# Performance work log

Measured on AMD Instinct MI355X. Metric: run time of the kernel, lower is better.

The kernel has to match this reference:

```python
import jax, jax.numpy as jnp
import numpy as np

B, N, DIM = 4, 4096, 1024
HEADS, DIM_HEAD, M = 16, 64, 128
DIM_INNER = HEADS * DIM_HEAD
SCALE = DIM_HEAD ** -0.5


def setup_inputs() -> dict:
    key = jax.random.key(0)
    ks = jax.random.split(key, 7)
    x = jax.random.normal(ks[0], (B, N, DIM), dtype=jnp.float32)
    mask = jax.random.bernoulli(ks[1], 0.9, (B, N))  # bool [b, n]
    W_qkv = jax.random.normal(ks[2], (DIM, 3 * DIM_INNER), dtype=jnp.float32) * (DIM ** -0.5)
    agent_tokens = jax.random.normal(ks[3], (HEADS, M, DIM_HEAD), dtype=jnp.float32) * 0.02
    W_qa = jax.random.normal(ks[4], (HEADS, HEADS), dtype=jnp.float32) * (HEADS ** -0.5)
    W_ak = jax.random.normal(ks[5], (HEADS, HEADS), dtype=jnp.float32) * (HEADS ** -0.5)
    W_out = jax.random.normal(ks[6], (DIM_INNER, DIM), dtype=jnp.float32) * (DIM_INNER ** -0.5)
    return {"x": x, "mask": mask, "W_qkv": W_qkv, "agent_tokens": agent_tokens,
            "W_qa": W_qa, "W_ak": W_ak, "W_out": W_out}


def reference(x, mask, W_qkv, agent_tokens, W_qa, W_ak, W_out):
    b, n, _ = x.shape
    h, m, d = agent_tokens.shape
    # qkv projection -> [3, b, h, n, d]  (layout matches 'b n (qkv h d)')
    qkv = (x @ W_qkv).reshape(b, n, 3, h, d).transpose(2, 0, 3, 1, 4)
    q, k, v = qkv[0], qkv[1], qkv[2]
    a = agent_tokens * SCALE  # [h, m, d]
    # stage 1: query-agent similarities [b, h, n, m]
    qa_sim = jnp.einsum('bhid,hjd->bhij', q, a)
    # stage 2: agent-key similarities [b, h, m, n]
    ak_sim = jnp.einsum('hid,bhjd->bhij', a, k)
    max_neg = -jnp.finfo(ak_sim.dtype).max
    ak_sim = jnp.where(mask[:, None, None, :], ak_sim, max_neg)
    qa_attn = jax.nn.softmax(qa_sim, axis=-1)
    ak_attn = jax.nn.softmax(ak_sim, axis=-1)
    # talking heads: 1x1 conv over head dim == head-mixing matmul
    qa_attn = jnp.einsum('gh,bhij->bgij', W_qa, qa_attn)
    ak_attn = jnp.einsum('gh,bhij->bgij', W_ak, ak_attn)
    agent_out = jnp.einsum('bhmn,bhnd->bhmd', ak_attn, v)    # [b, h, m, d]
    out = jnp.einsum('bhnm,bhmd->bhnd', qa_attn, agent_out)  # [b, h, n, d]
    out = jnp.where(mask[:, None, :, None], out, 0.0)
    out = out.transpose(0, 2, 1, 3).reshape(b, n, h * d)
    return out @ W_out
```

## Files before the change

kernel.cpp:

```cpp
#include <hip/hip_runtime.h>
#include <stdint.h>

#define DEVI __device__ __forceinline__

typedef __bf16 bf16x8 __attribute__((ext_vector_type(8)));
typedef float  f32x4  __attribute__((ext_vector_type(4)));
typedef unsigned int u32x2 __attribute__((ext_vector_type(2)));
typedef unsigned int u32x4 __attribute__((ext_vector_type(4)));


DEVI unsigned short f2bf(float f) {
  union { float f; unsigned int u; } c; c.f = f;
  return (unsigned short)((c.u + 0x7fffu + ((c.u >> 16) & 1u)) >> 16);
}
DEVI float bf2f(unsigned short s) {
  union { unsigned int u; float f; } c; c.u = ((unsigned int)s) << 16;
  return c.f;
}
DEVI u32x2 pack4(float a, float b, float c, float d) {
  u32x2 r;
  r.x = (unsigned)f2bf(a) | ((unsigned)f2bf(b) << 16);
  r.y = (unsigned)f2bf(c) | ((unsigned)f2bf(d) << 16);
  return r;
}
DEVI bf16x8 ldg8(const unsigned short* p) { return *(const bf16x8*)p; }

DEVI void g2l16(const void* g, void* l) {
  __builtin_amdgcn_global_load_lds(
      (const __attribute__((address_space(1))) unsigned int*)g,
      (__attribute__((address_space(3))) unsigned int*)l, 16, 0, 0);
}

#define MFMA16(acc, a, b) acc = __builtin_amdgcn_mfma_f32_16x16x32_bf16((a), (b), (acc), 0, 0, 0)

__global__ __launch_bounds__(256) void k_prep(
    const float* __restrict__ x, const float* __restrict__ Wqkv,
    const float* __restrict__ ag, const float* __restrict__ Wout,
    unsigned short* __restrict__ Xb, unsigned short* __restrict__ WqkvT,
    unsigned short* __restrict__ Ab, unsigned short* __restrict__ WoT)
{
  __shared__ float ldsT[32][33];
  const int tid = threadIdx.x;
  int bx = blockIdx.x;
  if (bx < 16384) {
    size_t i4 = ((size_t)bx * 256 + tid) * 4;
    f32x4 v = *(const f32x4*)&x[i4];
    *(u32x2*)&Xb[i4] = pack4(v[0], v[1], v[2], v[3]);
    return;
  }
  bx -= 16384;
  if (bx < 3072) {
    int jt = bx % 96, kt = bx / 96;
    int r32 = tid >> 3, c4 = (tid & 7) * 4;
    f32x4 v = *(const f32x4*)&Wqkv[(size_t)(kt * 32 + r32) * 3072 + jt * 32 + c4];
#pragma unroll
    for (int i = 0; i < 4; i++) ldsT[r32][c4 + i] = v[i];
    __syncthreads();
    float o0 = ldsT[c4 + 0][r32], o1 = ldsT[c4 + 1][r32];
    float o2 = ldsT[c4 + 2][r32], o3 = ldsT[c4 + 3][r32];
    *(u32x2*)&WqkvT[(size_t)(jt * 32 + r32) * 1024 + kt * 32 + c4] = pack4(o0, o1, o2, o3);
    return;
  }
  bx -= 3072;
  if (bx < 128) {
    size_t i4 = ((size_t)bx * 256 + tid) * 4;
    f32x4 v = *(const f32x4*)&ag[i4];
    *(u32x2*)&Ab[i4] = pack4(v[0] * 0.125f, v[1] * 0.125f, v[2] * 0.125f, v[3] * 0.125f);
    return;
  }
  bx -= 128;
  {
    int ct = bx % 32, dt = bx / 32;
    int r32 = tid >> 3, c4 = (tid & 7) * 4;
    f32x4 v = *(const f32x4*)&Wout[(size_t)(dt * 32 + r32) * 1024 + ct * 32 + c4];
#pragma unroll
    for (int i = 0; i < 4; i++) ldsT[r32][c4 + i] = v[i];
    __syncthreads();
    float o0 = ldsT[c4 + 0][r32], o1 = ldsT[c4 + 1][r32];
    float o2 = ldsT[c4 + 2][r32], o3 = ldsT[c4 + 3][r32];
    *(u32x2*)&WoT[(size_t)(ct * 32 + r32) * 1024 + dt * 32 + c4] = pack4(o0, o1, o2, o3);
  }
}

__global__ __launch_bounds__(256, 2) void k_gemm_qkv(
    const unsigned short* __restrict__ A, const unsigned short* __restrict__ Bt,
    unsigned short* __restrict__ Q, unsigned short* __restrict__ Kd,
    unsigned short* __restrict__ Vt)
{
  __shared__ __align__(16) unsigned short lA[4096];
  __shared__ __align__(16) unsigned short lB[4096];
  const int tid = threadIdx.x, lane = tid & 63, w = tid >> 6;
  const int q = lane >> 4, r = lane & 15, wr = w >> 1, wc = w & 1;
  const int row0 = blockIdx.y * 128, col0 = blockIdx.x * 128;
  const bool qk = blockIdx.x < 16;
  const int c1 = w, c2 = w + 4;
  const int sr1 = c1 * 16 + (lane >> 2), sr2 = c2 * 16 + (lane >> 2);
  const int sk = 8 * (lane & 3);
  const unsigned short* gA1 = A + (size_t)(row0 + sr1) * 1024 + sk;
  const unsigned short* gA2 = A + (size_t)(row0 + sr2) * 1024 + sk;
  const unsigned short* gB1 = Bt + (size_t)(col0 + sr1) * 1024 + sk;
  const unsigned short* gB2 = Bt + (size_t)(col0 + sr2) * 1024 + sk;
  const unsigned short* sA = qk ? lB : lA;
  const unsigned short* sB = qk ? lA : lB;
  f32x4 acc[4][4];
  const f32x4 z = {0.f, 0.f, 0.f, 0.f};
#pragma unroll
  for (int i = 0; i < 4; i++)
#pragma unroll
    for (int j = 0; j < 4; j++) acc[i][j] = z;

  for (int k0 = 0; k0 < 1024; k0 += 32) {
    g2l16(gA1 + k0, &lA[c1 * 512]);
    g2l16(gA2 + k0, &lA[c2 * 512]);
    g2l16(gB1 + k0, &lB[c1 * 512]);
    g2l16(gB2 + k0, &lB[c2 * 512]);
    __syncthreads();
    bf16x8 af[4], bv[4];
#pragma unroll
    for (int rt = 0; rt < 4; rt++) af[rt] = *(const bf16x8*)&sA[(64 * wr + 16 * rt + r) * 32 + q * 8];
#pragma unroll
    for (int ct = 0; ct < 4; ct++) bv[ct] = *(const bf16x8*)&sB[(64 * wc + 16 * ct + r) * 32 + q * 8];
#pragma unroll
    for (int rt = 0; rt < 4; rt++)
#pragma unroll
      for (int ct = 0; ct < 4; ct++) MFMA16(acc[rt][ct], af[rt], bv[ct]);
    __syncthreads();
  }
  const int b = row0 >> 12;
  if (qk) {
    unsigned short* dst = (blockIdx.x < 8) ? Q : Kd;
    const int hbase = ((col0 & 1023) >> 6) + wr;
#pragma unroll
    for (int rt = 0; rt < 4; rt++)
#pragma unroll
      for (int ct = 0; ct < 4; ct++) {
        int d0 = 16 * rt + 4 * q;
        int n = (row0 & 4095) + 64 * wc + 16 * ct + r;
        u32x2 pk = pack4(acc[rt][ct][0], acc[rt][ct][1], acc[rt][ct][2], acc[rt][ct][3]);
        *(u32x2*)&dst[(((size_t)(b * 16 + hbase)) * 4096 + n) * 64 + d0] = pk;
      }
  } else {
#pragma unroll
    for (int rt = 0; rt < 4; rt++)
#pragma unroll
      for (int ct = 0; ct < 4; ct++) {
        int j = (col0 - 2048) + 64 * wc + 16 * ct + r;
        int h = j >> 6, d = j & 63;
        int nb = (row0 & 4095) + 64 * wr + 16 * rt + 4 * q;
        u32x2 pk = pack4(acc[rt][ct][0], acc[rt][ct][1], acc[rt][ct][2], acc[rt][ct][3]);
        *(u32x2*)&Vt[(((size_t)(b * 16 + h)) * 64 + d) * 4096 + nb] = pk;
      }
  }
}

__global__ __launch_bounds__(256, 2) void k_qa(
    const unsigned short* __restrict__ Q, const unsigned short* __restrict__ Ab,
    unsigned short* __restrict__ QA)
{
  const int tid = threadIdx.x, lane = tid & 63, w = tid >> 6;
  const int q = lane >> 4, r = lane & 15, wr = w >> 1, wc = w & 1;
  const int nt = blockIdx.x, h = blockIdx.y, b = blockIdx.z;
  const unsigned short* Qb = Q + (((size_t)(b * 16 + h)) * 4096 + nt * 128) * 64;
  const unsigned short* Ah = Ab + (size_t)h * 8192;
  f32x4 acc[4][4];
  const f32x4 z = {0.f, 0.f, 0.f, 0.f};
#pragma unroll
  for (int i = 0; i < 4; i++)
#pragma unroll
    for (int j = 0; j < 4; j++) acc[i][j] = z;
#pragma unroll
  for (int ks = 0; ks < 2; ks++) {
    bf16x8 af[4], bv[4];
#pragma unroll
    for (int rt = 0; rt < 4; rt++) af[rt] = ldg8(Ah + (size_t)(64 * wr + 16 * rt + r) * 64 + ks * 32 + q * 8);
#pragma unroll
    for (int ct = 0; ct < 4; ct++) bv[ct] = ldg8(Qb + (size_t)(64 * wc + 16 * ct + r) * 64 + ks * 32 + q * 8);
#pragma unroll
    for (int rt = 0; rt < 4; rt++)
#pragma unroll
      for (int ct = 0; ct < 4; ct++) MFMA16(acc[rt][ct], af[rt], bv[ct]);
  }
  __shared__ float rs[2][128];
  float cs[4];
#pragma unroll
  for (int ct = 0; ct < 4; ct++) {
    float s = 0.f;
#pragma unroll
    for (int rt = 0; rt < 4; rt++)
#pragma unroll
      for (int reg = 0; reg < 4; reg++) {
        float e = __expf(acc[rt][ct][reg]);
        acc[rt][ct][reg] = e; s += e;
      }
    s += __shfl_xor(s, 16); s += __shfl_xor(s, 32);
    cs[ct] = s;
  }
  if (q == 0) {
#pragma unroll
    for (int ct = 0; ct < 4; ct++) rs[wr][64 * wc + 16 * ct + r] = cs[ct];
  }
  __syncthreads();
#pragma unroll
  for (int ct = 0; ct < 4; ct++) {
    int nl = 64 * wc + 16 * ct + r;
    float inv = 1.0f / (rs[0][nl] + rs[1][nl]);
    int n = nt * 128 + nl;
    size_t base = (((size_t)(b * 16 + h)) * 4096 + n) * 128;
#pragma unroll
    for (int rt = 0; rt < 4; rt++) {
      int m0 = 64 * wr + 16 * rt + 4 * q;
      u32x2 pk = pack4(acc[rt][ct][0] * inv, acc[rt][ct][1] * inv,
                       acc[rt][ct][2] * inv, acc[rt][ct][3] * inv);
      *(u32x2*)&QA[base + m0] = pk;
    }
  }
}

__global__ __launch_bounds__(256, 2) void k_ak(
    const unsigned short* __restrict__ Kd, const unsigned short* __restrict__ Ab,
    const int* __restrict__ mask, unsigned short* __restrict__ E, float* __restrict__ rowsum)
{
  const int tid = threadIdx.x, lane = tid & 63, w = tid >> 6;
  const int q = lane >> 4, r = lane & 15, wr = w >> 1, wc = w & 1;
  const int nt = blockIdx.x, h = blockIdx.y, b = blockIdx.z;
  const unsigned short* Kb = Kd + (((size_t)(b * 16 + h)) * 4096 + nt * 128) * 64;
  const unsigned short* Ah = Ab + (size_t)h * 8192;
  f32x4 acc[4][4];
  const f32x4 z = {0.f, 0.f, 0.f, 0.f};
#pragma unroll
  for (int i = 0; i < 4; i++)
#pragma unroll
    for (int j = 0; j < 4; j++) acc[i][j] = z;
#pragma unroll
  for (int ks = 0; ks < 2; ks++) {
    bf16x8 af[4], bv[4];
#pragma unroll
    for (int rt = 0; rt < 4; rt++) af[rt] = ldg8(Kb + (size_t)(64 * wr + 16 * rt + r) * 64 + ks * 32 + q * 8);
#pragma unroll
    for (int ct = 0; ct < 4; ct++) bv[ct] = ldg8(Ah + (size_t)(64 * wc + 16 * ct + r) * 64 + ks * 32 + q * 8);
#pragma unroll
    for (int rt = 0; rt < 4; rt++)
#pragma unroll
      for (int ct = 0; ct < 4; ct++) MFMA16(acc[rt][ct], af[rt], bv[ct]);
  }
  __shared__ float rs[2][128];
  float cs[4] = {0.f, 0.f, 0.f, 0.f};
#pragma unroll
  for (int rt = 0; rt < 4; rt++) {
    const int4 mkv = *(const int4*)&mask[b * 4096 + nt * 128 + 64 * wr + 16 * rt + 4 * q];
    int mka[4] = {mkv.x, mkv.y, mkv.z, mkv.w};
#pragma unroll
    for (int ct = 0; ct < 4; ct++) {
#pragma unroll
      for (int reg = 0; reg < 4; reg++) {
        float e = mka[reg] ? __expf(acc[rt][ct][reg]) : 0.0f;
        acc[rt][ct][reg] = e; cs[ct] += e;
      }
    }
  }
#pragma unroll
  for (int ct = 0; ct < 4; ct++) {
    float s = cs[ct];
    s += __shfl_xor(s, 16); s += __shfl_xor(s, 32);
    cs[ct] = s;
  }
  if (q == 0) {
#pragma unroll
    for (int ct = 0; ct < 4; ct++) rs[wr][64 * wc + 16 * ct + r] = cs[ct];
  }
#pragma unroll
  for (int ct = 0; ct < 4; ct++) {
    int m = 64 * wc + 16 * ct + r;
    size_t base = (((size_t)(b * 16 + h)) * 128 + m) * 4096;
#pragma unroll
    for (int rt = 0; rt < 4; rt++) {
      int n0 = nt * 128 + 64 * wr + 16 * rt + 4 * q;
      u32x2 pk = pack4(acc[rt][ct][0], acc[rt][ct][1], acc[rt][ct][2], acc[rt][ct][3]);
      *(u32x2*)&E[base + n0] = pk;
    }
  }
  __syncthreads();
  if (tid < 128) atomicAdd(&rowsum[(b * 16 + h) * 128 + tid], rs[0][tid] + rs[1][tid]);
}

__global__ __launch_bounds__(256) void k_mix(
    const unsigned short* __restrict__ E, const float* __restrict__ rowsum,
    const float* __restrict__ Wak, unsigned short* __restrict__ MIX)
{
  const int tid = threadIdx.x;
  const int m = blockIdx.y, b = blockIdx.z;
  __shared__ float wv[256];
  __shared__ float inv[16];
  wv[tid] = Wak[tid];
  if (tid < 16) inv[tid] = 1.0f / rowsum[(b * 16 + tid) * 128 + m];
  __syncthreads();
  const int n0 = (blockIdx.x * 256 + tid) * 4;
  float p[16][4];
#pragma unroll
  for (int h = 0; h < 16; h++) {
    u32x2 v = *(const u32x2*)&E[(((size_t)(b * 16 + h)) * 128 + m) * 4096 + n0];
    float iv = inv[h];
    p[h][0] = bf2f((unsigned short)(v.x & 0xffff)) * iv;
    p[h][1] = bf2f((unsigned short)(v.x >> 16)) * iv;
    p[h][2] = bf2f((unsigned short)(v.y & 0xffff)) * iv;
    p[h][3] = bf2f((unsigned short)(v.y >> 16)) * iv;
  }
#pragma unroll
  for (int g = 0; g < 16; g++) {
    float s0 = 0.f, s1 = 0.f, s2 = 0.f, s3 = 0.f;
#pragma unroll
    for (int h = 0; h < 16; h++) {
      float wgh = wv[g * 16 + h];
      s0 += wgh * p[h][0]; s1 += wgh * p[h][1]; s2 += wgh * p[h][2]; s3 += wgh * p[h][3];
    }
    *(u32x2*)&MIX[(((size_t)(b * 16 + g)) * 128 + m) * 4096 + n0] = pack4(s0, s1, s2, s3);
  }
}

__global__ __launch_bounds__(256) void k_ao(
    const unsigned short* __restrict__ MIX, const unsigned short* __restrict__ Vt,
    float* __restrict__ AO)
{
  const int tid = threadIdx.x, lane = tid & 63, w4 = tid >> 6;
  const int q = lane >> 4, r = lane & 15;
  const int kc = blockIdx.x, g = blockIdx.y, b = blockIdx.z;
  const unsigned short* Abase = MIX + ((size_t)(b * 16 + g)) * 128 * 4096;
  const unsigned short* Bbase = Vt + ((size_t)(b * 16 + g)) * 64 * 4096;
  f32x4 acc[2][4];
  const f32x4 z = {0.f, 0.f, 0.f, 0.f};
#pragma unroll
  for (int i = 0; i < 2; i++)
#pragma unroll
    for (int j = 0; j < 4; j++) acc[i][j] = z;
  for (int n = kc * 512; n < kc * 512 + 512; n += 32) {
    bf16x8 af[2], bv[4];
#pragma unroll
    for (int rt = 0; rt < 2; rt++) af[rt] = ldg8(Abase + (size_t)(32 * w4 + 16 * rt + r) * 4096 + n + q * 8);
#pragma unroll
    for (int ct = 0; ct < 4; ct++) bv[ct] = ldg8(Bbase + (size_t)(16 * ct + r) * 4096 + n + q * 8);
#pragma unroll
    for (int rt = 0; rt < 2; rt++)
#pragma unroll
      for (int ct = 0; ct < 4; ct++) MFMA16(acc[rt][ct], af[rt], bv[ct]);
  }
#pragma unroll
  for (int rt = 0; rt < 2; rt++)
#pragma unroll
    for (int ct = 0; ct < 4; ct++)
#pragma unroll
      for (int reg = 0; reg < 4; reg++) {
        int m = 32 * w4 + 16 * rt + 4 * q + reg, d = 16 * ct + r;
        atomicAdd(&AO[(((size_t)(b * 16 + g)) * 64 + d) * 128 + m], acc[rt][ct][reg]);
      }
}

__global__ __launch_bounds__(256) void k_mixqa(
    const unsigned short* __restrict__ QA, const float* __restrict__ Wqa,
    unsigned short* __restrict__ QAmix)
{
  const int tid = threadIdx.x;
  const int b = blockIdx.y;
  __shared__ float wv[256];
  wv[tid] = Wqa[tid];
  __syncthreads();
  const size_t i0 = ((size_t)blockIdx.x * 256 + tid) * 4;
  float p[16][4];
#pragma unroll
  for (int h = 0; h < 16; h++) {
    u32x2 v = *(const u32x2*)&QA[((size_t)(b * 16 + h)) * 524288 + i0];
    p[h][0] = bf2f((unsigned short)(v.x & 0xffff));
    p[h][1] = bf2f((unsigned short)(v.x >> 16));
    p[h][2] = bf2f((unsigned short)(v.y & 0xffff));
    p[h][3] = bf2f((unsigned short)(v.y >> 16));
  }
#pragma unroll
  for (int g = 0; g < 16; g++) {
    float s0 = 0.f, s1 = 0.f, s2 = 0.f, s3 = 0.f;
#pragma unroll
    for (int h = 0; h < 16; h++) {
      float wgh = wv[g * 16 + h];
      s0 += wgh * p[h][0]; s1 += wgh * p[h][1]; s2 += wgh * p[h][2]; s3 += wgh * p[h][3];
    }
    *(u32x2*)&QAmix[((size_t)(b * 16 + g)) * 524288 + i0] = pack4(s0, s1, s2, s3);
  }
}

__global__ __launch_bounds__(256) void k_o1(
    const unsigned short* __restrict__ QAmix, const float* __restrict__ AOt,
    unsigned short* __restrict__ out1)
{
  const int tid = threadIdx.x, lane = tid & 63, w4 = tid >> 6;
  const int q = lane >> 4, r = lane & 15;
  const int nt = blockIdx.x, g = blockIdx.y, b = blockIdx.z;
  const unsigned short* Bbase = QAmix + (((size_t)(b * 16 + g)) * 4096 + nt * 128) * 128;
  const float* Abase = AOt + ((size_t)(b * 16 + g)) * 8192;
  f32x4 acc[4][2];
  const f32x4 z = {0.f, 0.f, 0.f, 0.f};
#pragma unroll
  for (int i = 0; i < 4; i++)
#pragma unroll
    for (int j = 0; j < 2; j++) acc[i][j] = z;
#pragma unroll
  for (int ks = 0; ks < 4; ks++) {
    bf16x8 af[4], bv[2];
#pragma unroll
    for (int rt = 0; rt < 4; rt++) {
      const float* p = Abase + (size_t)(16 * rt + r) * 128 + ks * 32 + q * 8;
      f32x4 f0 = *(const f32x4*)p;
      f32x4 f1 = *(const f32x4*)(p + 4);
      bf16x8 t;
#pragma unroll
      for (int jj = 0; jj < 4; jj++) { t[jj] = (__bf16)f0[jj]; t[4 + jj] = (__bf16)f1[jj]; }
      af[rt] = t;
    }
#pragma unroll
    for (int ct = 0; ct < 2; ct++)
      bv[ct] = ldg8(Bbase + (size_t)(32 * w4 + 16 * ct + r) * 128 + ks * 32 + q * 8);
#pragma unroll
    for (int rt = 0; rt < 4; rt++)
#pragma unroll
      for (int ct = 0; ct < 2; ct++) MFMA16(acc[rt][ct], af[rt], bv[ct]);
  }
#pragma unroll
  for (int ct = 0; ct < 2; ct++) {
    int n = nt * 128 + 32 * w4 + 16 * ct + r;
    size_t base = ((size_t)b * 4096 + n) * 1024 + g * 64;
#pragma unroll
    for (int rt = 0; rt < 4; rt++) {
      int d0 = 16 * rt + 4 * q;
      u32x2 pk = pack4(acc[rt][ct][0], acc[rt][ct][1], acc[rt][ct][2], acc[rt][ct][3]);
      *(u32x2*)&out1[base + d0] = pk;
    }
  }
}

__global__ __launch_bounds__(256, 2) void k_fin2(
    const unsigned short* __restrict__ A, const unsigned short* __restrict__ Bt,
    const int* __restrict__ mask, float* __restrict__ out)
{
  __shared__ __align__(16) unsigned short lA[4096];
  __shared__ __align__(16) unsigned short lB[4096];
  const int tid = threadIdx.x, lane = tid & 63, w = tid >> 6;
  const int q = lane >> 4, r = lane & 15, wr = w >> 1, wc = w & 1;
  const int row0 = blockIdx.y * 128, col0 = blockIdx.x * 128;
  const int c1 = w, c2 = w + 4;
  const int sr1 = c1 * 16 + (lane >> 2), sr2 = c2 * 16 + (lane >> 2);
  const int sk = 8 * (lane & 3);
  const unsigned short* gA1 = A + (size_t)(row0 + sr1) * 1024 + sk;
  const unsigned short* gA2 = A + (size_t)(row0 + sr2) * 1024 + sk;
  const unsigned short* gB1 = Bt + (size_t)(col0 + sr1) * 1024 + sk;
  const unsigned short* gB2 = Bt + (size_t)(col0 + sr2) * 1024 + sk;
  f32x4 acc[4][4];
  const f32x4 z = {0.f, 0.f, 0.f, 0.f};
#pragma unroll
  for (int i = 0; i < 4; i++)
#pragma unroll
    for (int j = 0; j < 4; j++) acc[i][j] = z;
  for (int k0 = 0; k0 < 1024; k0 += 32) {
    g2l16(gA1 + k0, &lA[c1 * 512]);
    g2l16(gA2 + k0, &lA[c2 * 512]);
    g2l16(gB1 + k0, &lB[c1 * 512]);
    g2l16(gB2 + k0, &lB[c2 * 512]);
    __syncthreads();
    bf16x8 af[4], bv[4];
#pragma unroll
    for (int rt = 0; rt < 4; rt++) af[rt] = *(const bf16x8*)&lA[(64 * wr + 16 * rt + r) * 32 + q * 8];
#pragma unroll
    for (int ct = 0; ct < 4; ct++) bv[ct] = *(const bf16x8*)&lB[(64 * wc + 16 * ct + r) * 32 + q * 8];
#pragma unroll
    for (int rt = 0; rt < 4; rt++)
#pragma unroll
      for (int ct = 0; ct < 4; ct++) MFMA16(acc[rt][ct], af[rt], bv[ct]);
    __syncthreads();
  }
#pragma unroll
  for (int rt = 0; rt < 4; rt++)
#pragma unroll
    for (int reg = 0; reg < 4; reg++) {
      int row = row0 + 64 * wr + 16 * rt + 4 * q + reg;
      int mv = mask[row];
#pragma unroll
      for (int ct = 0; ct < 4; ct++) {
        int c = col0 + 64 * wc + 16 * ct + r;
        out[(size_t)row * 1024 + c] = mv ? acc[rt][ct][reg] : 0.0f;
      }
    }
}

extern "C" void kernel_launch(void* const* d_in, const int* in_sizes, int n_in,
                              void* d_out, int out_size, void* d_ws, size_t ws_size,
                              hipStream_t stream) {
  const float* x    = (const float*)d_in[0];
  const int*   mask = (const int*)d_in[1];
  const float* Wqkv = (const float*)d_in[2];
  const float* ag   = (const float*)d_in[3];
  const float* Wqa  = (const float*)d_in[4];
  const float* Wak  = (const float*)d_in[5];
  const float* Wout = (const float*)d_in[6];
  float* out = (float*)d_out;
  char* ws = (char*)d_ws;

  unsigned short* QA    = (unsigned short*)(ws + 0);
  unsigned short* QQ    = (unsigned short*)(ws + 67108864);
  unsigned short* KK    = (unsigned short*)(ws + 67108864 + 33554432);
  unsigned short* MIX   = QQ;
  unsigned short* out1  = QQ;
  unsigned short* VT    = (unsigned short*)(ws + 134217728);
  unsigned short* Xb    = (unsigned short*)(ws + 167772160);
  unsigned short* WqkvT = (unsigned short*)(ws + 167772160 + 33554432);
  unsigned short* E     = Xb;
  unsigned short* QAmix = Xb;
  char* sm = ws + 234881024;
  unsigned short* Ab  = (unsigned short*)(sm);
  unsigned short* WoT = (unsigned short*)(sm + 262144);
  float* rowsum = (float*)(sm + 262144 + 2097152);
  float* AOt    = (float*)(sm + 262144 + 2097152 + 32768);

  hipMemsetAsync(rowsum, 0, 4 * 16 * 128 * 4, stream);
  hipMemsetAsync(AOt, 0, 4 * 16 * 128 * 64 * 4, stream);

  k_prep<<<20608, 256, 0, stream>>>(x, Wqkv, ag, Wout, Xb, WqkvT, Ab, WoT);
  k_gemm_qkv<<<dim3(24, 128), 256, 0, stream>>>(Xb, WqkvT, QQ, KK, VT);
  k_qa<<<dim3(32, 16, 4), 256, 0, stream>>>(QQ, Ab, QA);
  k_ak<<<dim3(32, 16, 4), 256, 0, stream>>>(KK, Ab, mask, E, rowsum);
  k_mix<<<dim3(4, 128, 4), 256, 0, stream>>>(E, rowsum, Wak, MIX);
  k_ao<<<dim3(8, 16, 4), 256, 0, stream>>>(MIX, VT, AOt);
  k_mixqa<<<dim3(512, 4), 256, 0, stream>>>(QA, Wqa, QAmix);
  k_o1<<<dim3(32, 16, 4), 256, 0, stream>>>(QAmix, AOt, out1);
  k_fin2<<<dim3(8, 128), 256, 0, stream>>>(out1, WoT, mask, out);
}
```

Baseline: 547.2 us.

## Fuse qa/ak kernels, replace atomics with partial-sum reduction, swap grid order

Merges the query-agent and agent-key softmax kernels into one launch and folds the rowsum zeroing into the prep kernel, removing two memsets and one launch. The agent-output kernel now writes per-chunk partial sums to scratch, and a new reduction kernel adds them, replacing scalar float atomics. The two GEMM grids are transposed so consecutive blocks walk rows and share the same weight tile, which may change L2 reuse. In exchange it adds an extra launch, a scratch buffer and more register pressure in the fused kernel.

```diff
diff --git a/kernel.cpp b/kernel.cpp
--- a/kernel.cpp
+++ b/kernel.cpp
@@ -6,7 +6,6 @@
 typedef __bf16 bf16x8 __attribute__((ext_vector_type(8)));
 typedef float  f32x4  __attribute__((ext_vector_type(4)));
 typedef unsigned int u32x2 __attribute__((ext_vector_type(2)));
-typedef unsigned int u32x4 __attribute__((ext_vector_type(4)));
 
 
 DEVI unsigned short f2bf(float f) {
@@ -37,7 +36,8 @@
     const float* __restrict__ x, const float* __restrict__ Wqkv,
     const float* __restrict__ ag, const float* __restrict__ Wout,
     unsigned short* __restrict__ Xb, unsigned short* __restrict__ WqkvT,
-    unsigned short* __restrict__ Ab, unsigned short* __restrict__ WoT)
+    unsigned short* __restrict__ Ab, unsigned short* __restrict__ WoT,
+    float* __restrict__ rowsum)
 {
   __shared__ float ldsT[32][33];
   const int tid = threadIdx.x;
@@ -69,7 +69,7 @@
     return;
   }
   bx -= 128;
-  {
+  if (bx < 1024) {
     int ct = bx % 32, dt = bx / 32;
     int r32 = tid >> 3, c4 = (tid & 7) * 4;
     f32x4 v = *(const f32x4*)&Wout[(size_t)(dt * 32 + r32) * 1024 + ct * 32 + c4];
@@ -79,6 +79,12 @@
     float o0 = ldsT[c4 + 0][r32], o1 = ldsT[c4 + 1][r32];
     float o2 = ldsT[c4 + 2][r32], o3 = ldsT[c4 + 3][r32];
     *(u32x2*)&WoT[(size_t)(ct * 32 + r32) * 1024 + dt * 32 + c4] = pack4(o0, o1, o2, o3);
+    return;
+  }
+  bx -= 1024;
+  {
+    const f32x4 z = {0.f, 0.f, 0.f, 0.f};
+    *(f32x4*)&rowsum[((size_t)bx * 256 + tid) * 4] = z;
   }
 }
 
@@ -91,8 +97,8 @@
   __shared__ __align__(16) unsigned short lB[4096];
   const int tid = threadIdx.x, lane = tid & 63, w = tid >> 6;
   const int q = lane >> 4, r = lane & 15, wr = w >> 1, wc = w & 1;
-  const int row0 = blockIdx.y * 128, col0 = blockIdx.x * 128;
-  const bool qk = blockIdx.x < 16;
+  const int row0 = blockIdx.x * 128, col0 = blockIdx.y * 128;
+  const bool qk = blockIdx.y < 16;
   const int c1 = w, c2 = w + 4;
   const int sr1 = c1 * 16 + (lane >> 2), sr2 = c2 * 16 + (lane >> 2);
   const int sk = 8 * (lane & 3);
@@ -128,7 +134,7 @@
   }
   const int b = row0 >> 12;
   if (qk) {
-    unsigned short* dst = (blockIdx.x < 8) ? Q : Kd;
+    unsigned short* dst = (blockIdx.y < 8) ? Q : Kd;
     const int hbase = ((col0 & 1023) >> 6) + wr;
 #pragma unroll
     for (int rt = 0; rt < 4; rt++)
@@ -153,134 +159,131 @@
   }
 }
 
-__global__ __launch_bounds__(256, 2) void k_qa(
-    const unsigned short* __restrict__ Q, const unsigned short* __restrict__ Ab,
-    unsigned short* __restrict__ QA)
+__global__ __launch_bounds__(256, 2) void k_qk(
+    const unsigned short* __restrict__ Q, const unsigned short* __restrict__ Kd,
+    const unsigned short* __restrict__ Ab, const int* __restrict__ mask,
+    unsigned short* __restrict__ QA, unsigned short* __restrict__ E,
+    float* __restrict__ rowsum)
 {
   const int tid = threadIdx.x, lane = tid & 63, w = tid >> 6;
   const int q = lane >> 4, r = lane & 15, wr = w >> 1, wc = w & 1;
   const int nt = blockIdx.x, h = blockIdx.y, b = blockIdx.z;
   const unsigned short* Qb = Q + (((size_t)(b * 16 + h)) * 4096 + nt * 128) * 64;
-  const unsigned short* Ah = Ab + (size_t)h * 8192;
-  f32x4 acc[4][4];
-  const f32x4 z = {0.f, 0.f, 0.f, 0.f};
-#pragma unroll
-  for (int i = 0; i < 4; i++)
-#pragma unroll
-    for (int j = 0; j < 4; j++) acc[i][j] = z;
-#pragma unroll
-  for (int ks = 0; ks < 2; ks++) {
-    bf16x8 af[4], bv[4];
-#pragma unroll
-    for (int rt = 0; rt < 4; rt++) af[rt] = ldg8(Ah + (size_t)(64 * wr + 16 * rt + r) * 64 + ks * 32 + q * 8);
-#pragma unroll
-    for (int ct = 0; ct < 4; ct++) bv[ct] = ldg8(Qb + (size_t)(64 * wc + 16 * ct + r) * 64 + ks * 32 + q * 8);
-#pragma unroll
-    for (int rt = 0; rt < 4; rt++)
-#pragma unroll
-      for (int ct = 0; ct < 4; ct++) MFMA16(acc[rt][ct], af[rt], bv[ct]);
-  }
-  __shared__ float rs[2][128];
-  float cs[4];
-#pragma unroll
-  for (int ct = 0; ct < 4; ct++) {
-    float s = 0.f;
-#pragma unroll
-    for (int rt = 0; rt < 4; rt++)
-#pragma unroll
-      for (int reg = 0; reg < 4; reg++) {
-        float e = __expf(acc[rt][ct][reg]);
-        acc[rt][ct][reg] = e; s += e;
-      }
-    s += __shfl_xor(s, 16); s += __shfl_xor(s, 32);
-    cs[ct] = s;
-  }
-  if (q == 0) {
-#pragma unroll
-    for (int ct = 0; ct < 4; ct++) rs[wr][64 * wc + 16 * ct + r] = cs[ct];
-  }
-  __syncthreads();
-#pragma unroll
-  for (int ct = 0; ct < 4; ct++) {
-    int nl = 64 * wc + 16 * ct + r;
-    float inv = 1.0f / (rs[0][nl] + rs[1][nl]);
-    int n = nt * 128 + nl;
-    size_t base = (((size_t)(b * 16 + h)) * 4096 + n) * 128;
-#pragma unroll
-    for (int rt = 0; rt < 4; rt++) {
-      int m0 = 64 * wr + 16 * rt + 4 * q;
-      u32x2 pk = pack4(acc[rt][ct][0] * inv, acc[rt][ct][1] * inv,
-                       acc[rt][ct][2] * inv, acc[rt][ct][3] * inv);
-      *(u32x2*)&QA[base + m0] = pk;
-    }
-  }
-}
-
-__global__ __launch_bounds__(256, 2) void k_ak(
-    const unsigned short* __restrict__ Kd, const unsigned short* __restrict__ Ab,
-    const int* __restrict__ mask, unsigned short* __restrict__ E, float* __restrict__ rowsum)
-{
-  const int tid = threadIdx.x, lane = tid & 63, w = tid >> 6;
-  const int q = lane >> 4, r = lane & 15, wr = w >> 1, wc = w & 1;
-  const int nt = blockIdx.x, h = blockIdx.y, b = blockIdx.z;
   const unsigned short* Kb = Kd + (((size_t)(b * 16 + h)) * 4096 + nt * 128) * 64;
   const unsigned short* Ah = Ab + (size_t)h * 8192;
-  f32x4 acc[4][4];
+  __shared__ float rs[2][128];
   const f32x4 z = {0.f, 0.f, 0.f, 0.f};
-#pragma unroll
-  for (int i = 0; i < 4; i++)
-#pragma unroll
-    for (int j = 0; j < 4; j++) acc[i][j] = z;
-#pragma unroll
-  for (int ks = 0; ks < 2; ks++) {
-    bf16x8 af[4], bv[4];
-#pragma unroll
-    for (int rt = 0; rt < 4; rt++) af[rt] = ldg8(Kb + (size_t)(64 * wr + 16 * rt + r) * 64 + ks * 32 + q * 8);
-#pragma unroll
-    for (int ct = 0; ct < 4; ct++) bv[ct] = ldg8(Ah + (size_t)(64 * wc + 16 * ct + r) * 64 + ks * 32 + q * 8);
-#pragma unroll
-    for (int rt = 0; rt < 4; rt++)
-#pragma unroll
-      for (int ct = 0; ct < 4; ct++) MFMA16(acc[rt][ct], af[rt], bv[ct]);
-  }
-  __shared__ float rs[2][128];
-  float cs[4] = {0.f, 0.f, 0.f, 0.f};
-#pragma unroll
-  for (int rt = 0; rt < 4; rt++) {
-    const int4 mkv = *(const int4*)&mask[b * 4096 + nt * 128 + 64 * wr + 16 * rt + 4 * q];
-    int mka[4] = {mkv.x, mkv.y, mkv.z, mkv.w};
+
+  {
+    f32x4 acc[4][4];
+#pragma unroll
+    for (int i = 0; i < 4; i++)
+#pragma unroll
+      for (int j = 0; j < 4; j++) acc[i][j] = z;
+#pragma unroll
+    for (int ks = 0; ks < 2; ks++) {
+      bf16x8 af[4], bv[4];
+#pragma unroll
+      for (int rt = 0; rt < 4; rt++) af[rt] = ldg8(Ah + (size_t)(64 * wr + 16 * rt + r) * 64 + ks * 32 + q * 8);
+#pragma unroll
+      for (int ct = 0; ct < 4; ct++) bv[ct] = ldg8(Qb + (size_t)(64 * wc + 16 * ct + r) * 64 + ks * 32 + q * 8);
+#pragma unroll
+      for (int rt = 0; rt < 4; rt++)
+#pragma unroll
+        for (int ct = 0; ct < 4; ct++) MFMA16(acc[rt][ct], af[rt], bv[ct]);
+    }
+    float cs[4];
 #pragma unroll
     for (int ct = 0; ct < 4; ct++) {
-#pragma unroll
-      for (int reg = 0; reg < 4; reg++) {
-        float e = mka[reg] ? __expf(acc[rt][ct][reg]) : 0.0f;
-        acc[rt][ct][reg] = e; cs[ct] += e;
+      float s = 0.f;
+#pragma unroll
+      for (int rt = 0; rt < 4; rt++)
+#pragma unroll
+        for (int reg = 0; reg < 4; reg++) {
+          float e = __expf(acc[rt][ct][reg]);
+          acc[rt][ct][reg] = e; s += e;
+        }
+      s += __shfl_xor(s, 16); s += __shfl_xor(s, 32);
+      cs[ct] = s;
+    }
+    if (q == 0) {
+#pragma unroll
+      for (int ct = 0; ct < 4; ct++) rs[wr][64 * wc + 16 * ct + r] = cs[ct];
+    }
+    __syncthreads();
+#pragma unroll
+    for (int ct = 0; ct < 4; ct++) {
+      int nl = 64 * wc + 16 * ct + r;
+      float inv = 1.0f / (rs[0][nl] + rs[1][nl]);
+      int n = nt * 128 + nl;
+      size_t base = (((size_t)(b * 16 + h)) * 4096 + n) * 128;
+#pragma unroll
+      for (int rt = 0; rt < 4; rt++) {
+        int m0 = 64 * wr + 16 * rt + 4 * q;
+        u32x2 pk = pack4(acc[rt][ct][0] * inv, acc[rt][ct][1] * inv,
+                         acc[rt][ct][2] * inv, acc[rt][ct][3] * inv);
+        *(u32x2*)&QA[base + m0] = pk;
       }
     }
   }
-#pragma unroll
-  for (int ct = 0; ct < 4; ct++) {
-    float s = cs[ct];
-    s += __shfl_xor(s, 16); s += __shfl_xor(s, 32);
-    cs[ct] = s;
-  }
-  if (q == 0) {
-#pragma unroll
-    for (int ct = 0; ct < 4; ct++) rs[wr][64 * wc + 16 * ct + r] = cs[ct];
-  }
-#pragma unroll
-  for (int ct = 0; ct < 4; ct++) {
-    int m = 64 * wc + 16 * ct + r;
-    size_t base = (((size_t)(b * 16 + h)) * 128 + m) * 4096;
+  __syncthreads();
+
+  {
+    f32x4 acc[4][4];
+#pragma unroll
+    for (int i = 0; i < 4; i++)
+#pragma unroll
+      for (int j = 0; j < 4; j++) acc[i][j] = z;
+#pragma unroll
+    for (int ks = 0; ks < 2; ks++) {
+      bf16x8 af[4], bv[4];
+#pragma unroll
+      for (int rt = 0; rt < 4; rt++) af[rt] = ldg8(Kb + (size_t)(64 * wr + 16 * rt + r) * 64 + ks * 32 + q * 8);
+#pragma unroll
+      for (int ct = 0; ct < 4; ct++) bv[ct] = ldg8(Ah + (size_t)(64 * wc + 16 * ct + r) * 64 + ks * 32 + q * 8);
+#pragma unroll
+      for (int rt = 0; rt < 4; rt++)
+#pragma unroll
+        for (int ct = 0; ct < 4; ct++) MFMA16(acc[rt][ct], af[rt], bv[ct]);
+    }
+    float cs[4] = {0.f, 0.f, 0.f, 0.f};
 #pragma unroll
     for (int rt = 0; rt < 4; rt++) {
-      int n0 = nt * 128 + 64 * wr + 16 * rt + 4 * q;
-      u32x2 pk = pack4(acc[rt][ct][0], acc[rt][ct][1], acc[rt][ct][2], acc[rt][ct][3]);
-      *(u32x2*)&E[base + n0] = pk;
-    }
-  }
-  __syncthreads();
-  if (tid < 128) atomicAdd(&rowsum[(b * 16 + h) * 128 + tid], rs[0][tid] + rs[1][tid]);
+      const int4 mkv = *(const int4*)&mask[b * 4096 + nt * 128 + 64 * wr + 16 * rt + 4 * q];
+      int mka[4] = {mkv.x, mkv.y, mkv.z, mkv.w};
+#pragma unroll
+      for (int ct = 0; ct < 4; ct++) {
+#pragma unroll
+        for (int reg = 0; reg < 4; reg++) {
+          float e = mka[reg] ? __expf(acc[rt][ct][reg]) : 0.0f;
+          acc[rt][ct][reg] = e; cs[ct] += e;
+        }
+      }
+    }
+#pragma unroll
+    for (int ct = 0; ct < 4; ct++) {
+      float s = cs[ct];
+      s += __shfl_xor(s, 16); s += __shfl_xor(s, 32);
+      cs[ct] = s;
+    }
+    if (q == 0) {
+#pragma unroll
+      for (int ct = 0; ct < 4; ct++) rs[wr][64 * wc + 16 * ct + r] = cs[ct];
+    }
+#pragma unroll
+    for (int ct = 0; ct < 4; ct++) {
+      int m = 64 * wc + 16 * ct + r;
+      size_t base = (((size_t)(b * 16 + h)) * 128 + m) * 4096;
+#pragma unroll
+      for (int rt = 0; rt < 4; rt++) {
+        int n0 = nt * 128 + 64 * wr + 16 * rt + 4 * q;
+        u32x2 pk = pack4(acc[rt][ct][0], acc[rt][ct][1], acc[rt][ct][2], acc[rt][ct][3]);
+        *(u32x2*)&E[base + n0] = pk;
+      }
+    }
+    __syncthreads();
+    if (tid < 128) atomicAdd(&rowsum[(b * 16 + h) * 128 + tid], rs[0][tid] + rs[1][tid]);
+  }
 }
 
 __global__ __launch_bounds__(256) void k_mix(
@@ -319,7 +322,7 @@
 
 __global__ __launch_bounds__(256) void k_ao(
     const unsigned short* __restrict__ MIX, const unsigned short* __restrict__ Vt,
-    float* __restrict__ AO)
+    float* __restrict__ P)
 {
   const int tid = threadIdx.x, lane = tid & 63, w4 = tid >> 6;
   const int q = lane >> 4, r = lane & 15;
@@ -343,15 +346,27 @@
 #pragma unroll
       for (int ct = 0; ct < 4; ct++) MFMA16(acc[rt][ct], af[rt], bv[ct]);
   }
+  float* Pp = P + (size_t)kc * 524288 + ((size_t)(b * 16 + g)) * 8192;
 #pragma unroll
   for (int rt = 0; rt < 2; rt++)
 #pragma unroll
-    for (int ct = 0; ct < 4; ct++)
-#pragma unroll
-      for (int reg = 0; reg < 4; reg++) {
-        int m = 32 * w4 + 16 * rt + 4 * q + reg, d = 16 * ct + r;
-        atomicAdd(&AO[(((size_t)(b * 16 + g)) * 64 + d) * 128 + m], acc[rt][ct][reg]);
-      }
+    for (int ct = 0; ct < 4; ct++) {
+      int m0 = 32 * w4 + 16 * rt + 4 * q, d = 16 * ct + r;
+      *(f32x4*)&Pp[(size_t)d * 128 + m0] = acc[rt][ct];
+    }
+}
+
+__global__ __launch_bounds__(256) void k_aored(
+    const float* __restrict__ P, float* __restrict__ AOt)
+{
+  size_t i = ((size_t)blockIdx.x * 256 + threadIdx.x) * 4;
+  f32x4 s = *(const f32x4*)&P[i];
+#pragma unroll
+  for (int kc = 1; kc < 8; kc++) {
+    f32x4 v = *(const f32x4*)&P[(size_t)kc * 524288 + i];
+    s[0] += v[0]; s[1] += v[1]; s[2] += v[2]; s[3] += v[3];
+  }
+  *(f32x4*)&AOt[i] = s;
 }
 
 __global__ __launch_bounds__(256) void k_mixqa(
@@ -442,7 +457,7 @@
   __shared__ __align__(16) unsigned short lB[4096];
   const int tid = threadIdx.x, lane = tid & 63, w = tid >> 6;
   const int q = lane >> 4, r = lane & 15, wr = w >> 1, wc = w & 1;
-  const int row0 = blockIdx.y * 128, col0 = blockIdx.x * 128;
+  const int row0 = blockIdx.x * 128, col0 = blockIdx.y * 128;
   const int c1 = w, c2 = w + 4;
   const int sr1 = c1 * 16 + (lane >> 2), sr2 = c2 * 16 + (lane >> 2);
   const int sk = 8 * (lane & 3);
@@ -509,6 +524,7 @@
   unsigned short* Xb    = (unsigned short*)(ws + 167772160);
   unsigned short* WqkvT = (unsigned short*)(ws + 167772160 + 33554432);
   unsigned short* E     = Xb;
+  float*          Ppart = (float*)Xb;
   unsigned short* QAmix = Xb;
   char* sm = ws + 234881024;
   unsigned short* Ab  = (unsigned short*)(sm);
@@ -516,16 +532,13 @@
   float* rowsum = (float*)(sm + 262144 + 2097152);
   float* AOt    = (float*)(sm + 262144 + 2097152 + 32768);
 
-  hipMemsetAsync(rowsum, 0, 4 * 16 * 128 * 4, stream);
-  hipMemsetAsync(AOt, 0, 4 * 16 * 128 * 64 * 4, stream);
-
-  k_prep<<<20608, 256, 0, stream>>>(x, Wqkv, ag, Wout, Xb, WqkvT, Ab, WoT);
-  k_gemm_qkv<<<dim3(24, 128), 256, 0, stream>>>(Xb, WqkvT, QQ, KK, VT);
-  k_qa<<<dim3(32, 16, 4), 256, 0, stream>>>(QQ, Ab, QA);
-  k_ak<<<dim3(32, 16, 4), 256, 0, stream>>>(KK, Ab, mask, E, rowsum);
+  k_prep<<<20616, 256, 0, stream>>>(x, Wqkv, ag, Wout, Xb, WqkvT, Ab, WoT, rowsum);
+  k_gemm_qkv<<<dim3(128, 24), 256, 0, stream>>>(Xb, WqkvT, QQ, KK, VT);
+  k_qk<<<dim3(32, 16, 4), 256, 0, stream>>>(QQ, KK, Ab, mask, QA, E, rowsum);
   k_mix<<<dim3(4, 128, 4), 256, 0, stream>>>(E, rowsum, Wak, MIX);
-  k_ao<<<dim3(8, 16, 4), 256, 0, stream>>>(MIX, VT, AOt);
+  k_ao<<<dim3(8, 16, 4), 256, 0, stream>>>(MIX, VT, Ppart);
+  k_aored<<<512, 256, 0, stream>>>(Ppart, AOt);
   k_mixqa<<<dim3(512, 4), 256, 0, stream>>>(QA, Wqa, QAmix);
   k_o1<<<dim3(32, 16, 4), 256, 0, stream>>>(QAmix, AOt, out1);
-  k_fin2<<<dim3(8, 128), 256, 0, stream>>>(out1, WoT, mask, out);
-}
+  k_fin2<<<dim3(128, 8), 256, 0, stream>>>(out1, WoT, mask, out);
+}
```

Measured after the change: 493.2 us. -9.9%, faster.
